# Kernel optimization log

Measured on AMD Instinct MI355X. Metric: run time of the kernel, lower is better.

## Reference

```python
import jax, jax.numpy as jnp
import numpy as np

B, T, S, D, H, DK = 2, 2048, 2048, 1024, 16, 64


def setup_inputs() -> dict:
    key = jax.random.key(0)
    ks = jax.random.split(key, 11)
    s = 1.0 / np.sqrt(D)
    return {
        "query": jax.random.normal(ks[0], (B, T, D), jnp.float32),
        "value": jax.random.normal(ks[1], (B, S, D), jnp.float32),
        "key": jax.random.normal(ks[2], (B, S, D), jnp.float32),
        "Wq": jax.random.normal(ks[3], (D, H, DK), jnp.float32) * s,
        "bq": jnp.zeros((H, DK), jnp.float32),
        "Wk": jax.random.normal(ks[4], (D, H, DK), jnp.float32) * s,
        "bk": jnp.zeros((H, DK), jnp.float32),
        "Wv": jax.random.normal(ks[5], (D, H, DK), jnp.float32) * s,
        "bv": jnp.zeros((H, DK), jnp.float32),
        "Wo": jax.random.normal(ks[6], (H, DK, D), jnp.float32) * (1.0 / np.sqrt(H * DK)),
        "bo": jnp.zeros((D,), jnp.float32),
    }


def reference(query, value, key, Wq, bq, Wk, bk, Wv, bv, Wo, bo):
    # Projections: (B, seq, D) x (D, H, DK) -> (B, seq, H, DK)
    q = jnp.einsum("btd,dhk->bthk", query, Wq) + bq
    k = jnp.einsum("bsd,dhk->bshk", key, Wk) + bk
    v = jnp.einsum("bsd,dhk->bshk", value, Wv) + bv
    # Scaled dot-product attention (keras scales query by 1/sqrt(key_dim))
    q = q * (1.0 / np.sqrt(DK)).astype(np.float32)
    scores = jnp.einsum("bshk,bthk->bhts", k, q)  # (B, H, T, S)
    probs = jax.nn.softmax(scores, axis=-1)
    attn = jnp.einsum("bhts,bshk->bthk", probs, v)  # (B, T, H, DK)
    # Output projection back to model dim
    out = jnp.einsum("bthk,hkd->btd", attn, Wo) + bo
    return out
```

## Files before the change

kernel.cpp:

```cpp
#include <hip/hip_runtime.h>
#include <math.h>

#define BB  2
#define TT  2048
#define SSQ 2048
#define DD  1024
#define HH  16
#define DKK 64
#define MM  (BB*TT)
#define NN  (HH*DKK)

typedef __attribute__((ext_vector_type(8))) short short8;
typedef __attribute__((ext_vector_type(4))) float f32x4;
typedef __attribute__((ext_vector_type(2))) unsigned int uint2v;
typedef __attribute__((ext_vector_type(4))) unsigned int u32x4;

__device__ __forceinline__ short f2bf(float x) {
    unsigned u = __builtin_bit_cast(unsigned, x);
    unsigned r = (u + 0x7FFFu + ((u >> 16) & 1u)) >> 16;
    return (short)r;
}

__device__ __forceinline__ unsigned pk2(float lo, float hi) {
    return (__builtin_bit_cast(unsigned, hi) & 0xFFFF0000u) |
           (__builtin_bit_cast(unsigned, lo) >> 16);
}

__device__ __forceinline__ void glds16(const void* g, void* l) {
    __builtin_amdgcn_global_load_lds(
        (const __attribute__((address_space(1))) void*)g,
        (__attribute__((address_space(3))) void*)l, 16, 0, 0);
}

__global__ __launch_bounds__(256)
void prep(const float* __restrict__ aq, const float* __restrict__ ak,
          const float* __restrict__ av,
          const float* __restrict__ w0, const float* __restrict__ w1,
          const float* __restrict__ w2, const float* __restrict__ w3,
          short* __restrict__ oq, short* __restrict__ ok,
          short* __restrict__ ov,
          short* __restrict__ t0, short* __restrict__ t1,
          short* __restrict__ t2, short* __restrict__ t3)
{
    __shared__ float Ls[64][65];
    const int id = blockIdx.x;
    const int tid = threadIdx.x;

    if (id < 6144) {
        const int z = id >> 11;
        const int x = id & 2047;
        const float* in = (z == 0) ? aq : (z == 1) ? ak : av;
        short* out = (z == 0) ? oq : (z == 1) ? ok : ov;
        size_t i0 = ((size_t)x * 256 + tid) * 8;
        f32x4 f0 = *(const f32x4*)(in + i0);
        f32x4 f1 = *(const f32x4*)(in + i0 + 4);
        short8 v;
#pragma unroll
        for (int j = 0; j < 4; j++) v[j] = f2bf(f0[j]);
#pragma unroll
        for (int j = 0; j < 4; j++) v[4 + j] = f2bf(f1[j]);
        *(short8*)(out + i0) = v;
    } else {
        const int wid = id - 6144;
        const int z = wid >> 8;
        const int rem = wid & 255;
        const float* in = (z == 0) ? w0 : (z == 1) ? w1 : (z == 2) ? w2 : w3;
        short* out = (z == 0) ? t0 : (z == 1) ? t1 : (z == 2) ? t2 : t3;
        const int c0 = (rem & 15) * 64, r0 = (rem >> 4) * 64;
        const int r = tid >> 2, c4 = tid & 3;

        const float* src = in + (size_t)(r0 + r) * DD + c0 + c4 * 16;
#pragma unroll
        for (int i = 0; i < 4; i++) {
            f32x4 f = *(const f32x4*)(src + i * 4);
#pragma unroll
            for (int j = 0; j < 4; j++) Ls[r][c4 * 16 + i * 4 + j] = f[j];
        }
        __syncthreads();

        short8 va, vb;
#pragma unroll
        for (int j = 0; j < 8; j++) va[j] = f2bf(Ls[c4 * 16 + j][r]);
#pragma unroll
        for (int j = 0; j < 8; j++) vb[j] = f2bf(Ls[c4 * 16 + 8 + j][r]);
        short* dst = out + (size_t)(c0 + r) * DD + r0 + c4 * 16;
        *(short8*)dst = va;
        *(short8*)(dst + 8) = vb;
    }
}

__global__ __launch_bounds__(256, 3)
void gemm_qkv(const short* __restrict__ Aq, const short* __restrict__ Ak,
              const short* __restrict__ Av,
              const short* __restrict__ Wqt, const short* __restrict__ Wkt,
              const short* __restrict__ Wvt,
              const float* __restrict__ bq, const float* __restrict__ bk,
              const float* __restrict__ bv,
              short* __restrict__ Qb, short* __restrict__ Kb,
              short* __restrict__ Vbt)
{
    __shared__ short As[2][128 * 32];
    __shared__ short Bs[2][128 * 32];

    const int d = blockIdx.x + 8 * blockIdx.y + 256 * blockIdx.z;
    const int kx = d & 7, j = d >> 3;
    const int z = j >> 5;
    const int n0 = ((j >> 2) & 7) * 128;
    const int m0 = (4 * kx + (j & 3)) * 128;

    const short* A  = (z == 0) ? Aq : (z == 1) ? Ak : Av;
    const short* Bt = (z == 0) ? Wqt : (z == 1) ? Wkt : Wvt;
    const float* bias = (z == 0) ? bq : (z == 1) ? bk : bv;

    const int tid = threadIdx.x;
    const int w = tid >> 6, l = tid & 63;
    const int l15 = l & 15, quad = l >> 4;
    const int wm = w >> 1, wn = w & 1;
    const int r = tid >> 2, cseg = tid & 3;

    f32x4 acc[4][4];
#pragma unroll
    for (int i = 0; i < 4; i++)
#pragma unroll
        for (int jj = 0; jj < 4; jj++) acc[i][jj] = (f32x4){0.f, 0.f, 0.f, 0.f};

    const short* gA = A + (size_t)(m0 + r) * DD + cseg * 8;
    const short* gB = Bt + (size_t)(n0 + r) * DD + cseg * 8;

    glds16(gA + 0,               &As[0][w * 512]);
    glds16(gA + (size_t)64 * DD, &As[0][2048 + w * 512]);
    glds16(gB + 0,               &Bs[0][w * 512]);
    glds16(gB + (size_t)64 * DD, &Bs[0][2048 + w * 512]);

    for (int k0 = 0; k0 < DD; k0 += 32) {
        const int cur = (k0 >> 5) & 1;
        __syncthreads();
        if (k0 + 32 < DD) {
            glds16(gA + k0 + 32,                   &As[cur ^ 1][w * 512]);
            glds16(gA + (size_t)64 * DD + k0 + 32, &As[cur ^ 1][2048 + w * 512]);
            glds16(gB + k0 + 32,                   &Bs[cur ^ 1][w * 512]);
            glds16(gB + (size_t)64 * DD + k0 + 32, &Bs[cur ^ 1][2048 + w * 512]);
        }

        short8 bF[4];
#pragma unroll
        for (int ni = 0; ni < 4; ni++)
            bF[ni] = *(const short8*)&Bs[cur][(wn * 64 + ni * 16 + l15) * 32 + quad * 8];
        if (z != 2) {
#pragma unroll
            for (int mi = 0; mi < 4; mi++) {
                short8 aF = *(const short8*)&As[cur][(wm * 64 + mi * 16 + l15) * 32 + quad * 8];
#pragma unroll
                for (int ni = 0; ni < 4; ni++)
                    acc[mi][ni] = __builtin_amdgcn_mfma_f32_16x16x32_bf16(aF, bF[ni], acc[mi][ni], 0, 0, 0);
            }
        } else {
#pragma unroll
            for (int mi = 0; mi < 4; mi++) {
                short8 aF = *(const short8*)&As[cur][(wm * 64 + mi * 16 + l15) * 32 + quad * 8];
#pragma unroll
                for (int ni = 0; ni < 4; ni++)
                    acc[ni][mi] = __builtin_amdgcn_mfma_f32_16x16x32_bf16(bF[ni], aF, acc[ni][mi], 0, 0, 0);
            }
        }
    }

    if (z != 2) {
        short* dst = (z == 0) ? Qb : Kb;
        const float scale = (z == 0) ? 0.1803368801f : 1.0f;
#pragma unroll
        for (int mi = 0; mi < 4; mi++) {
#pragma unroll
            for (int reg = 0; reg < 4; reg++) {
                int m = m0 + wm * 64 + mi * 16 + quad * 4 + reg;
                int b = m >> 11, t = m & 2047;
#pragma unroll
                for (int ni = 0; ni < 4; ni++) {
                    int n = n0 + wn * 64 + ni * 16 + l15;
                    float vv = (acc[mi][ni][reg] + bias[n]) * scale;
                    int h = n >> 6, dk = n & 63;
                    dst[((size_t)(b * HH + h) * TT + t) * DKK + dk] = f2bf(vv);
                }
            }
        }
    } else {
        const int b = m0 >> 11;
        const int tl0 = (m0 & 2047) + wm * 64;
#pragma unroll
        for (int ni = 0; ni < 4; ni++) {
#pragma unroll
            for (int reg = 0; reg < 4; reg++) {
                int n = n0 + wn * 64 + ni * 16 + quad * 4 + reg;
                int h = n >> 6, dk = n & 63;
                float bb = bias[n];
                short* vrow = Vbt + ((size_t)(b * HH + h) * DKK + dk) * SSQ;
#pragma unroll
                for (int mi = 0; mi < 4; mi++) {
                    int t = tl0 + mi * 16 + l15;
                    vrow[t] = f2bf(acc[ni][mi][reg] + bb);
                }
            }
        }
    }
}

__global__ __launch_bounds__(256, 4)
void gemm_out(const short* __restrict__ Ab, const short* __restrict__ Wot,
              const float* __restrict__ bo, float* __restrict__ out)
{
    __shared__ short As[2][2 * 64 * 32];
    __shared__ short Bs[2][2 * 64 * 32];

    const int d = blockIdx.x;
    const int kx = d & 7, j = d >> 3;
    const int m0 = (8 * kx + (j & 7)) * 64;
    const int n0 = (j >> 3) * 64;

    const int tid = threadIdx.x;
    const int w = tid >> 6, l = tid & 63;
    const int l15 = l & 15, quad = l >> 4;
    const int wm = w >> 1, wn = w & 1;

    f32x4 acc[2][2];
#pragma unroll
    for (int i = 0; i < 2; i++)
#pragma unroll
        for (int jj = 0; jj < 2; jj++) acc[i][jj] = (f32x4){0.f, 0.f, 0.f, 0.f};

    const int r = tid >> 2, cseg = tid & 3;
    const short* gA = Ab + (size_t)(m0 + r) * DD + cseg * 8;
    const short* gB = Wot + (size_t)(n0 + r) * DD + cseg * 8;

#define STAGE_OUT(buf, k0)                                        \
    do {                                                          \
        glds16(gA + (k0),      &As[buf][w * 512]);                \
        glds16(gA + (k0) + 32, &As[buf][2048 + w * 512]);         \
        glds16(gB + (k0),      &Bs[buf][w * 512]);                \
        glds16(gB + (k0) + 32, &Bs[buf][2048 + w * 512]);         \
    } while (0)

    STAGE_OUT(0, 0);

    for (int k0 = 0; k0 < DD; k0 += 64) {
        const int cur = (k0 >> 6) & 1;
        __syncthreads();
        if (k0 + 64 < DD) STAGE_OUT(cur ^ 1, k0 + 64);

#pragma unroll
        for (int kk = 0; kk < 2; kk++) {
            short8 bF[2];
#pragma unroll
            for (int ni = 0; ni < 2; ni++)
                bF[ni] = *(const short8*)&Bs[cur][kk * 2048 + (wn * 32 + ni * 16 + l15) * 32 + quad * 8];
#pragma unroll
            for (int mi = 0; mi < 2; mi++) {
                short8 aF = *(const short8*)&As[cur][kk * 2048 + (wm * 32 + mi * 16 + l15) * 32 + quad * 8];
#pragma unroll
                for (int ni = 0; ni < 2; ni++)
                    acc[mi][ni] = __builtin_amdgcn_mfma_f32_16x16x32_bf16(aF, bF[ni], acc[mi][ni], 0, 0, 0);
            }
        }
    }
#undef STAGE_OUT

#pragma unroll
    for (int mi = 0; mi < 2; mi++) {
#pragma unroll
        for (int reg = 0; reg < 4; reg++) {
            int m = m0 + wm * 32 + mi * 16 + quad * 4 + reg;
#pragma unroll
            for (int ni = 0; ni < 2; ni++) {
                int n = n0 + wn * 32 + ni * 16 + l15;
                out[(size_t)m * DD + n] = acc[mi][ni][reg] + bo[n];
            }
        }
    }
}

__global__ __launch_bounds__(256, 3)
void attn_mfma(const short* __restrict__ Qb, const short* __restrict__ Kb,
               const short* __restrict__ Vbt, short* __restrict__ Ab)
{
    __shared__ short KV[2 * 2 * 64 * 72];

    const int tid = threadIdx.x;
    const int w = tid >> 6, l = tid & 63;
    const int l15 = l & 15, quad = l >> 4;

    const int fid = blockIdx.y * 16 + blockIdx.x;
    const int swz = (fid & 7) * 64 + (fid >> 3);
    const int t0 = (swz & 15) * 128;
    const int bh = swz >> 4;
    const size_t hb = (size_t)bh * SSQ * DKK;
    const int r = tid >> 2, c4 = tid & 3;

    short8 qf[2][2];
#pragma unroll
    for (int mf = 0; mf < 2; mf++)
#pragma unroll
        for (int kk = 0; kk < 2; kk++)
            qf[mf][kk] = *(const short8*)(Qb + hb +
                (size_t)(t0 + 32 * w + 16 * mf + l15) * DKK + kk * 32 + quad * 8);

    const short* gkb = Kb + hb + (size_t)r * DKK + c4 * 16;
    const short* gvb = Vbt + hb + (size_t)r * SSQ + c4 * 16;
    short8 kr0 = *(const short8*)(gkb + 0);
    short8 kr1 = *(const short8*)(gkb + 8);
    short8 vr0 = *(const short8*)(gvb + 0);
    short8 vr1 = *(const short8*)(gvb + 8);

    f32x4 o[2][4];
#pragma unroll
    for (int mf = 0; mf < 2; mf++)
#pragma unroll
        for (int j = 0; j < 4; j++) o[mf][j] = (f32x4){0.f, 0.f, 0.f, 0.f};
    f32x4 lacc[2] = {(f32x4){0.f, 0.f, 0.f, 0.f}, (f32x4){0.f, 0.f, 0.f, 0.f}};
    const short8 ones = {(short)0x3F80, (short)0x3F80, (short)0x3F80, (short)0x3F80,
                         (short)0x3F80, (short)0x3F80, (short)0x3F80, (short)0x3F80};

    short* skb = KV + r * 72 + c4 * 16;

    for (int s0 = 0; s0 < SSQ; s0 += 64) {
        const int dbo = (s0 & 64) ? 9216 : 0;
        *(short8*)(skb + dbo)          = kr0;
        *(short8*)(skb + dbo + 8)      = kr1;
        *(short8*)(skb + dbo + 4608)   = vr0;
        *(short8*)(skb + dbo + 4616)   = vr1;
        if (s0 + 64 < SSQ) {
            const short* gk = gkb + (size_t)(s0 + 64) * DKK;
            const short* gv = gvb + (s0 + 64);
            kr0 = *(const short8*)(gk + 0);
            kr1 = *(const short8*)(gk + 8);
            vr0 = *(const short8*)(gv + 0);
            vr1 = *(const short8*)(gv + 8);
        }
        __syncthreads();
        const short* kb_ = KV + dbo;
        const short* vb_ = kb_ + 4608;

        f32x4 sc[4][2];
#pragma unroll
        for (int np = 0; np < 4; np++)
#pragma unroll
            for (int mf = 0; mf < 2; mf++) sc[np][mf] = (f32x4){0.f, 0.f, 0.f, 0.f};
        __builtin_amdgcn_s_setprio(1);
#pragma unroll
        for (int kk = 0; kk < 2; kk++) {
#pragma unroll
            for (int np = 0; np < 4; np++) {
                short8 aK = *(const short8*)&kb_[(16 * np + l15) * 72 + kk * 32 + quad * 8];
                sc[np][0] = __builtin_amdgcn_mfma_f32_16x16x32_bf16(aK, qf[0][kk], sc[np][0], 0, 0, 0);
                sc[np][1] = __builtin_amdgcn_mfma_f32_16x16x32_bf16(aK, qf[1][kk], sc[np][1], 0, 0, 0);
            }
        }
        __builtin_amdgcn_s_setprio(0);

        short8 pa[2][2];
#pragma unroll
        for (int mf = 0; mf < 2; mf++) {
#pragma unroll
            for (int kk = 0; kk < 2; kk++) {
                u32x4 wd;
#pragma unroll
                for (int b = 0; b < 2; b++) {
                    float p00 = __builtin_amdgcn_exp2f(sc[2 * kk][mf][2 * b]);
                    float p01 = __builtin_amdgcn_exp2f(sc[2 * kk][mf][2 * b + 1]);
                    float p10 = __builtin_amdgcn_exp2f(sc[2 * kk + 1][mf][2 * b]);
                    float p11 = __builtin_amdgcn_exp2f(sc[2 * kk + 1][mf][2 * b + 1]);
                    unsigned Xw = pk2(p00, p01);
                    unsigned Yw = pk2(p10, p11);
                    uint2v s1 = __builtin_amdgcn_permlane32_swap(Xw, Yw, false, false);
                    uint2v s2 = __builtin_amdgcn_permlane16_swap(s1[0], s1[1], false, false);
                    wd[b]     = s2[0];
                    wd[2 + b] = s2[1];
                }
                pa[mf][kk] = __builtin_bit_cast(short8, wd);
            }
        }

        __builtin_amdgcn_s_setprio(1);
#pragma unroll
        for (int kk = 0; kk < 2; kk++) {
            lacc[0] = __builtin_amdgcn_mfma_f32_16x16x32_bf16(pa[0][kk], ones, lacc[0], 0, 0, 0);
            lacc[1] = __builtin_amdgcn_mfma_f32_16x16x32_bf16(pa[1][kk], ones, lacc[1], 0, 0, 0);
#pragma unroll
            for (int np = 0; np < 4; np++) {
                short8 bV = *(const short8*)&vb_[(16 * np + l15) * 72 + kk * 32 + quad * 8];
                o[0][np] = __builtin_amdgcn_mfma_f32_16x16x32_bf16(pa[0][kk], bV, o[0][np], 0, 0, 0);
                o[1][np] = __builtin_amdgcn_mfma_f32_16x16x32_bf16(pa[1][kk], bV, o[1][np], 0, 0, 0);
            }
        }
        __builtin_amdgcn_s_setprio(0);
    }

    const int b = bh >> 4, h = bh & 15;
#pragma unroll
    for (int mf = 0; mf < 2; mf++) {
#pragma unroll
        for (int reg = 0; reg < 4; reg++) {
            float inv = 1.f / lacc[mf][reg];
            int t = t0 + 32 * w + 16 * mf + quad * 4 + reg;
#pragma unroll
            for (int np = 0; np < 4; np++) {
                Ab[((size_t)(b * TT + t) * HH + h) * DKK + 16 * np + l15] =
                    f2bf(o[mf][np][reg] * inv);
            }
        }
    }
}

extern "C" void kernel_launch(void* const* d_in, const int* in_sizes, int n_in,
                              void* d_out, int out_size, void* d_ws, size_t ws_size,
                              hipStream_t stream)
{
    const float* query = (const float*)d_in[0];
    const float* value = (const float*)d_in[1];
    const float* key   = (const float*)d_in[2];
    const float* Wq    = (const float*)d_in[3];
    const float* bq    = (const float*)d_in[4];
    const float* Wk    = (const float*)d_in[5];
    const float* bk    = (const float*)d_in[6];
    const float* Wv    = (const float*)d_in[7];
    const float* bv    = (const float*)d_in[8];
    const float* Wo    = (const float*)d_in[9];
    const float* bo    = (const float*)d_in[10];
    float* out = (float*)d_out;

    const size_t actE = (size_t)MM * DD;
    const size_t wE   = (size_t)DD * NN;
    short* p = (short*)d_ws;
    short* Aq   = p; p += actE;
    short* Ak   = p; p += actE;
    short* Av   = p; p += actE;
    short* Wqt  = p; p += wE;
    short* Wkt  = p; p += wE;
    short* Wvt  = p; p += wE;
    short* Wot  = p; p += wE;
    short* Qb   = p; p += actE;
    short* Kb   = p; p += actE;
    short* Vbt  = p; p += actE;
    short* Ab   = p; p += actE;

    dim3 blk(256);

    prep<<<dim3(7168), blk, 0, stream>>>(
        query, key, value, Wq, Wk, Wv, Wo, Aq, Ak, Av, Wqt, Wkt, Wvt, Wot);

    gemm_qkv<<<dim3(NN / 128, MM / 128, 3), blk, 0, stream>>>(
        Aq, Ak, Av, Wqt, Wkt, Wvt, bq, bk, bv, Qb, Kb, Vbt);

    attn_mfma<<<dim3(TT / 128, BB * HH), blk, 0, stream>>>(Qb, Kb, Vbt, Ab);

    gemm_out<<<dim3(1024), blk, 0, stream>>>(Ab, Wot, bo, out);
}
```

Before: 217.1 us.

## Fuse fp32-to-bf16 activation conversion into QKV GEMM LDS load path

Drops the separate activation conversion pass from the prep kernel. The QKV GEMM now stages fp32 activations straight into LDS through swizzled global_load_lds and converts them to bf16 with v_cvt_pk_bf16_f32 just before each MFMA. This saves a full write and re-read of three bf16 activation copies, but doubles A-tile LDS footprint and global bytes per K step inside the GEMM, and each A tile is re-read by 8 N-blocks, which may lower occupancy.

```diff
diff --git a/kernel.cpp b/kernel.cpp
--- a/kernel.cpp
+++ b/kernel.cpp
@@ -26,6 +26,17 @@
            (__builtin_bit_cast(unsigned, lo) >> 16);
 }
 
+__device__ __forceinline__ short8 cvt8(f32x4 x, f32x4 y) {
+    unsigned r0, r1, r2, r3;
+    asm("v_cvt_pk_bf16_f32 %0, %1, %2" : "=v"(r0) : "v"(x[0]), "v"(x[1]));
+    asm("v_cvt_pk_bf16_f32 %0, %1, %2" : "=v"(r1) : "v"(x[2]), "v"(x[3]));
+    asm("v_cvt_pk_bf16_f32 %0, %1, %2" : "=v"(r2) : "v"(y[0]), "v"(y[1]));
+    asm("v_cvt_pk_bf16_f32 %0, %1, %2" : "=v"(r3) : "v"(y[2]), "v"(y[3]));
+    u32x4 r;
+    r[0] = r0; r[1] = r1; r[2] = r2; r[3] = r3;
+    return __builtin_bit_cast(short8, r);
+}
+
 __device__ __forceinline__ void glds16(const void* g, void* l) {
     __builtin_amdgcn_global_load_lds(
         (const __attribute__((address_space(1))) void*)g,
@@ -33,65 +44,43 @@
 }
 
 __global__ __launch_bounds__(256)
-void prep(const float* __restrict__ aq, const float* __restrict__ ak,
-          const float* __restrict__ av,
-          const float* __restrict__ w0, const float* __restrict__ w1,
-          const float* __restrict__ w2, const float* __restrict__ w3,
-          short* __restrict__ oq, short* __restrict__ ok,
-          short* __restrict__ ov,
-          short* __restrict__ t0, short* __restrict__ t1,
-          short* __restrict__ t2, short* __restrict__ t3)
+void wprep(const float* __restrict__ w0, const float* __restrict__ w1,
+           const float* __restrict__ w2, const float* __restrict__ w3,
+           short* __restrict__ t0, short* __restrict__ t1,
+           short* __restrict__ t2, short* __restrict__ t3)
 {
     __shared__ float Ls[64][65];
     const int id = blockIdx.x;
     const int tid = threadIdx.x;
-
-    if (id < 6144) {
-        const int z = id >> 11;
-        const int x = id & 2047;
-        const float* in = (z == 0) ? aq : (z == 1) ? ak : av;
-        short* out = (z == 0) ? oq : (z == 1) ? ok : ov;
-        size_t i0 = ((size_t)x * 256 + tid) * 8;
-        f32x4 f0 = *(const f32x4*)(in + i0);
-        f32x4 f1 = *(const f32x4*)(in + i0 + 4);
-        short8 v;
-#pragma unroll
-        for (int j = 0; j < 4; j++) v[j] = f2bf(f0[j]);
-#pragma unroll
-        for (int j = 0; j < 4; j++) v[4 + j] = f2bf(f1[j]);
-        *(short8*)(out + i0) = v;
-    } else {
-        const int wid = id - 6144;
-        const int z = wid >> 8;
-        const int rem = wid & 255;
-        const float* in = (z == 0) ? w0 : (z == 1) ? w1 : (z == 2) ? w2 : w3;
-        short* out = (z == 0) ? t0 : (z == 1) ? t1 : (z == 2) ? t2 : t3;
-        const int c0 = (rem & 15) * 64, r0 = (rem >> 4) * 64;
-        const int r = tid >> 2, c4 = tid & 3;
-
-        const float* src = in + (size_t)(r0 + r) * DD + c0 + c4 * 16;
-#pragma unroll
-        for (int i = 0; i < 4; i++) {
-            f32x4 f = *(const f32x4*)(src + i * 4);
-#pragma unroll
-            for (int j = 0; j < 4; j++) Ls[r][c4 * 16 + i * 4 + j] = f[j];
-        }
-        __syncthreads();
-
-        short8 va, vb;
-#pragma unroll
-        for (int j = 0; j < 8; j++) va[j] = f2bf(Ls[c4 * 16 + j][r]);
-#pragma unroll
-        for (int j = 0; j < 8; j++) vb[j] = f2bf(Ls[c4 * 16 + 8 + j][r]);
-        short* dst = out + (size_t)(c0 + r) * DD + r0 + c4 * 16;
-        *(short8*)dst = va;
-        *(short8*)(dst + 8) = vb;
-    }
+    const int z = id >> 8;
+    const int rem = id & 255;
+    const float* in = (z == 0) ? w0 : (z == 1) ? w1 : (z == 2) ? w2 : w3;
+    short* out = (z == 0) ? t0 : (z == 1) ? t1 : (z == 2) ? t2 : t3;
+    const int c0 = (rem & 15) * 64, r0 = (rem >> 4) * 64;
+    const int r = tid >> 2, c4 = tid & 3;
+
+    const float* src = in + (size_t)(r0 + r) * DD + c0 + c4 * 16;
+#pragma unroll
+    for (int i = 0; i < 4; i++) {
+        f32x4 f = *(const f32x4*)(src + i * 4);
+#pragma unroll
+        for (int j = 0; j < 4; j++) Ls[r][c4 * 16 + i * 4 + j] = f[j];
+    }
+    __syncthreads();
+
+    short8 va, vb;
+#pragma unroll
+    for (int j = 0; j < 8; j++) va[j] = f2bf(Ls[c4 * 16 + j][r]);
+#pragma unroll
+    for (int j = 0; j < 8; j++) vb[j] = f2bf(Ls[c4 * 16 + 8 + j][r]);
+    short* dst = out + (size_t)(c0 + r) * DD + r0 + c4 * 16;
+    *(short8*)dst = va;
+    *(short8*)(dst + 8) = vb;
 }
 
 __global__ __launch_bounds__(256, 3)
-void gemm_qkv(const short* __restrict__ Aq, const short* __restrict__ Ak,
-              const short* __restrict__ Av,
+void gemm_qkv(const float* __restrict__ Aqf, const float* __restrict__ Akf,
+              const float* __restrict__ Avf,
               const short* __restrict__ Wqt, const short* __restrict__ Wkt,
               const short* __restrict__ Wvt,
               const float* __restrict__ bq, const float* __restrict__ bk,
@@ -99,7 +88,7 @@
               short* __restrict__ Qb, short* __restrict__ Kb,
               short* __restrict__ Vbt)
 {
-    __shared__ short As[2][128 * 32];
+    __shared__ float Af[2][128 * 32];
     __shared__ short Bs[2][128 * 32];
 
     const int d = blockIdx.x + 8 * blockIdx.y + 256 * blockIdx.z;
@@ -108,7 +97,7 @@
     const int n0 = ((j >> 2) & 7) * 128;
     const int m0 = (4 * kx + (j & 3)) * 128;
 
-    const short* A  = (z == 0) ? Aq : (z == 1) ? Ak : Av;
+    const float* A  = (z == 0) ? Aqf : (z == 1) ? Akf : Avf;
     const short* Bt = (z == 0) ? Wqt : (z == 1) ? Wkt : Wvt;
     const float* bias = (z == 0) ? bq : (z == 1) ? bk : bv;
 
@@ -124,32 +113,41 @@
 #pragma unroll
         for (int jj = 0; jj < 4; jj++) acc[i][jj] = (f32x4){0.f, 0.f, 0.f, 0.f};
 
-    const short* gA = A + (size_t)(m0 + r) * DD + cseg * 8;
+    const int arow_s = tid >> 3, aslot = tid & 7;
+    const int aswz = (aslot ^ (arow_s & 7)) * 4;
+    const float* gA = A + (size_t)(m0 + arow_s) * DD + aswz;
     const short* gB = Bt + (size_t)(n0 + r) * DD + cseg * 8;
 
-    glds16(gA + 0,               &As[0][w * 512]);
-    glds16(gA + (size_t)64 * DD, &As[0][2048 + w * 512]);
-    glds16(gB + 0,               &Bs[0][w * 512]);
-    glds16(gB + (size_t)64 * DD, &Bs[0][2048 + w * 512]);
+#define STAGE_QKV(buf, k0)                                                    \
+    do {                                                                      \
+        glds16(gA + (k0),                     &Af[buf][0 * 1024 + tid * 4]);  \
+        glds16(gA + (size_t)32 * DD + (k0),   &Af[buf][1 * 1024 + tid * 4]);  \
+        glds16(gA + (size_t)64 * DD + (k0),   &Af[buf][2 * 1024 + tid * 4]);  \
+        glds16(gA + (size_t)96 * DD + (k0),   &Af[buf][3 * 1024 + tid * 4]);  \
+        glds16(gB + (k0),                     &Bs[buf][w * 512]);             \
+        glds16(gB + (size_t)64 * DD + (k0),   &Bs[buf][2048 + w * 512]);      \
+    } while (0)
+
+    STAGE_QKV(0, 0);
 
     for (int k0 = 0; k0 < DD; k0 += 32) {
         const int cur = (k0 >> 5) & 1;
         __syncthreads();
-        if (k0 + 32 < DD) {
-            glds16(gA + k0 + 32,                   &As[cur ^ 1][w * 512]);
-            glds16(gA + (size_t)64 * DD + k0 + 32, &As[cur ^ 1][2048 + w * 512]);
-            glds16(gB + k0 + 32,                   &Bs[cur ^ 1][w * 512]);
-            glds16(gB + (size_t)64 * DD + k0 + 32, &Bs[cur ^ 1][2048 + w * 512]);
-        }
+        if (k0 + 32 < DD) STAGE_QKV(cur ^ 1, k0 + 32);
 
         short8 bF[4];
 #pragma unroll
         for (int ni = 0; ni < 4; ni++)
             bF[ni] = *(const short8*)&Bs[cur][(wn * 64 + ni * 16 + l15) * 32 + quad * 8];
+
         if (z != 2) {
 #pragma unroll
             for (int mi = 0; mi < 4; mi++) {
-                short8 aF = *(const short8*)&As[cur][(wm * 64 + mi * 16 + l15) * 32 + quad * 8];
+                const int arow = wm * 64 + mi * 16 + l15;
+                const int rx = (arow & 7);
+                f32x4 u = *(const f32x4*)&Af[cur][arow * 32 + ((quad * 2) ^ rx) * 4];
+                f32x4 v = *(const f32x4*)&Af[cur][arow * 32 + ((quad * 2 + 1) ^ rx) * 4];
+                short8 aF = cvt8(u, v);
 #pragma unroll
                 for (int ni = 0; ni < 4; ni++)
                     acc[mi][ni] = __builtin_amdgcn_mfma_f32_16x16x32_bf16(aF, bF[ni], acc[mi][ni], 0, 0, 0);
@@ -157,13 +155,18 @@
         } else {
 #pragma unroll
             for (int mi = 0; mi < 4; mi++) {
-                short8 aF = *(const short8*)&As[cur][(wm * 64 + mi * 16 + l15) * 32 + quad * 8];
+                const int arow = wm * 64 + mi * 16 + l15;
+                const int rx = (arow & 7);
+                f32x4 u = *(const f32x4*)&Af[cur][arow * 32 + ((quad * 2) ^ rx) * 4];
+                f32x4 v = *(const f32x4*)&Af[cur][arow * 32 + ((quad * 2 + 1) ^ rx) * 4];
+                short8 aF = cvt8(u, v);
 #pragma unroll
                 for (int ni = 0; ni < 4; ni++)
                     acc[ni][mi] = __builtin_amdgcn_mfma_f32_16x16x32_bf16(bF[ni], aF, acc[ni][mi], 0, 0, 0);
             }
         }
     }
+#undef STAGE_QKV
 
     if (z != 2) {
         short* dst = (z == 0) ? Qb : Kb;
@@ -429,9 +432,6 @@
     const size_t actE = (size_t)MM * DD;
     const size_t wE   = (size_t)DD * NN;
     short* p = (short*)d_ws;
-    short* Aq   = p; p += actE;
-    short* Ak   = p; p += actE;
-    short* Av   = p; p += actE;
     short* Wqt  = p; p += wE;
     short* Wkt  = p; p += wE;
     short* Wvt  = p; p += wE;
@@ -443,11 +443,10 @@
 
     dim3 blk(256);
 
-    prep<<<dim3(7168), blk, 0, stream>>>(
-        query, key, value, Wq, Wk, Wv, Wo, Aq, Ak, Av, Wqt, Wkt, Wvt, Wot);
+    wprep<<<dim3(1024), blk, 0, stream>>>(Wq, Wk, Wv, Wo, Wqt, Wkt, Wvt, Wot);
 
     gemm_qkv<<<dim3(NN / 128, MM / 128, 3), blk, 0, stream>>>(
-        Aq, Ak, Av, Wqt, Wkt, Wvt, bq, bk, bv, Qb, Kb, Vbt);
+        query, key, value, Wqt, Wkt, Wvt, bq, bk, bv, Qb, Kb, Vbt);
 
     attn_mfma<<<dim3(TT / 128, BB * HH), blk, 0, stream>>>(Qb, Kb, Vbt, Ab);
 
```

Result: no change. 217.8 us (+0.3%).
